# Performance work log

Hardware: AMD Instinct MI355X
Metric: run time of the kernel (lower is better)

Reference implementation:

```python
import jax, jax.numpy as jnp
import numpy as np

N = 100000      # nodes
DEG = 16        # fixed out-degree -> nnz = N*DEG (static for jit)
NNZ = N * DEG
IN_DIM, HID, OUT = 256, 64, 64


def setup_inputs() -> dict:
    key = jax.random.key(0)
    k1, k2, k3, k4, k5 = jax.random.split(key, 5)
    X = jax.random.normal(k1, (N, IN_DIM), dtype=jnp.float32)
    W1 = jax.random.normal(k2, (IN_DIM, HID), dtype=jnp.float32) / np.sqrt(IN_DIM)
    W2 = jax.random.normal(k3, (HID, OUT), dtype=jnp.float32) / np.sqrt(HID)
    vals = jax.random.uniform(k4, (NNZ,), dtype=jnp.float32)
    rowptr = (jnp.arange(N + 1, dtype=jnp.int32) * DEG)  # fixed-degree CSR
    colind = jax.random.randint(k5, (NNZ,), 0, N, dtype=jnp.int32)
    return {"X": X, "W1": W1, "W2": W2, "vals": vals,
            "rowptr": rowptr, "colind": colind}


def spmm_csr(rowptr, colind, vals, B):
    """CSR SpMM: out[i] = sum_{j in row i} vals[j] * B[colind[j]]."""
    deg = rowptr[1:] - rowptr[:-1]                      # [N]
    rows = jnp.repeat(jnp.arange(N, dtype=jnp.int32), deg,
                      total_repeat_length=NNZ)           # [NNZ]
    gathered = vals[:, None] * B[colind]                 # [NNZ, F]
    return jax.ops.segment_sum(gathered, rows, num_segments=N)


def reference(X, W1, W2, vals, rowptr, colind):
    h = X @ W1                        # lin1 (no bias)
    h = spmm_csr(rowptr, colind, vals, h)   # A @ h
    h = jax.nn.relu(h)
    out = h @ W2                      # lin2 (no bias)
    out = spmm_csr(rowptr, colind, vals, out)  # A @ out
    return out
```

## Files before the change

kernel.cpp:

```cpp
#include <hip/hip_runtime.h>
#include <hip/hip_bf16.h>

#define N_NODES 100000
#define DEG 16
#define NT16 6250
#define NG64 1563
#define G1_BLOCKS 782
#define G1_WSTRIDE (G1_BLOCKS * 4)

typedef __attribute__((ext_vector_type(8))) short short8;
typedef __attribute__((ext_vector_type(4))) float f32x4;
typedef __attribute__((ext_vector_type(4))) float f4raw;
typedef __attribute__((ext_vector_type(4))) int   i4raw;
typedef __attribute__((ext_vector_type(4))) unsigned u4raw;

__device__ inline unsigned short f2bf(float f) {
    union { float f; unsigned u; } v; v.f = f;
    unsigned u = v.u;
    u += 0x7FFFu + ((u >> 16) & 1u);
    return (unsigned short)(u >> 16);
}
__device__ inline unsigned pk2bf(float a, float b) {
    union { __hip_bfloat162 b2; unsigned u; } v;
    v.b2 = __float22bfloat162_rn(make_float2(a, b));
    return v.u;
}
__device__ inline float bflo(unsigned u) {
    union { unsigned u; float f; } v; v.u = u << 16; return v.f;
}
__device__ inline float bfhi(unsigned u) {
    union { unsigned u; float f; } v; v.u = u & 0xFFFF0000u; return v.f;
}

__global__ __launch_bounds__(256) void gemm1_k256(const float* __restrict__ X,
                                                  const float* __restrict__ W1,
                                                  unsigned short* __restrict__ h)
{
    __shared__ unsigned short wfrag[256 * 64];

    const int tid  = threadIdx.x;
    const int lane = tid & 63;
    const int wid  = tid >> 6;
    const int q    = lane >> 4;
    const int l16  = lane & 15;

    {
        const int kg = tid >> 2;
        const int cq = tid & 3;
        float4 wr[16];
        #pragma unroll
        for (int r = 0; r < 4; ++r)
            #pragma unroll
            for (int i = 0; i < 4; ++i)
                wr[r * 4 + i] = *(const float4*)(W1 + (kg * 4 + r) * 64 + cq * 16 + i * 4);
        const int kb  = kg >> 3;
        const int lnr = (((kg * 4) >> 3) & 3) * 16;
        const int jb  = (kg * 4) & 7;
        #pragma unroll
        for (int c = 0; c < 16; ++c) {
            ushort4 w4;
            #pragma unroll
            for (int r = 0; r < 4; ++r) {
                float4 v = wr[r * 4 + (c >> 2)];
                float  f = ((c & 3) == 0) ? v.x : ((c & 3) == 1) ? v.y :
                           ((c & 3) == 2) ? v.z : v.w;
                ((unsigned short*)&w4)[r] = f2bf(f);
            }
            *(ushort4*)&wfrag[(((kb * 4) + cq) * 64 + lnr + c) * 8 + jb] = w4;
        }
    }
    __syncthreads();

    const int bpidx = (((l16 << 2) | q) << 2);
    const size_t xoff = (size_t)(lane >> 2) * 256 + (lane & 3) * 8;

    int t = blockIdx.x * 4 + wid;

    f4raw pa[8];
    {
        const float* xb = X + (size_t)t * 16 * 256 + xoff;
        #pragma unroll
        for (int kb = 0; kb < 4; ++kb) {
            pa[2 * kb]     = __builtin_nontemporal_load((const f4raw*)(xb + kb * 32));
            pa[2 * kb + 1] = __builtin_nontemporal_load((const f4raw*)(xb + kb * 32 + 4));
        }
    }

    while (t < NT16) {
        const float* xb = X + (size_t)t * 16 * 256 + xoff;
        f4raw pb[8];
        #pragma unroll
        for (int kb = 4; kb < 8; ++kb) {
            pb[2 * (kb - 4)]     = __builtin_nontemporal_load((const f4raw*)(xb + kb * 32));
            pb[2 * (kb - 4) + 1] = __builtin_nontemporal_load((const f4raw*)(xb + kb * 32 + 4));
        }

        f32x4 a0 = {0,0,0,0}, a1 = {0,0,0,0}, a2 = {0,0,0,0}, a3 = {0,0,0,0};

        #pragma unroll
        for (int kb = 0; kb < 4; ++kb) {
            union { int u[4]; short8 s; } uu;
            uu.u[0] = __builtin_amdgcn_ds_bpermute(bpidx, (int)pk2bf(pa[2*kb].x,   pa[2*kb].y));
            uu.u[1] = __builtin_amdgcn_ds_bpermute(bpidx, (int)pk2bf(pa[2*kb].z,   pa[2*kb].w));
            uu.u[2] = __builtin_amdgcn_ds_bpermute(bpidx, (int)pk2bf(pa[2*kb+1].x, pa[2*kb+1].y));
            uu.u[3] = __builtin_amdgcn_ds_bpermute(bpidx, (int)pk2bf(pa[2*kb+1].z, pa[2*kb+1].w));
            const short8* wp = (const short8*)&wfrag[(size_t)((kb * 4) * 64 + lane) * 8];
            a0 = __builtin_amdgcn_mfma_f32_16x16x32_bf16(uu.s, wp[0 * 64], a0, 0, 0, 0);
            a1 = __builtin_amdgcn_mfma_f32_16x16x32_bf16(uu.s, wp[1 * 64], a1, 0, 0, 0);
            a2 = __builtin_amdgcn_mfma_f32_16x16x32_bf16(uu.s, wp[2 * 64], a2, 0, 0, 0);
            a3 = __builtin_amdgcn_mfma_f32_16x16x32_bf16(uu.s, wp[3 * 64], a3, 0, 0, 0);
        }

        const int tn = t + G1_WSTRIDE;
        if (tn < NT16) {
            const float* xn = X + (size_t)tn * 16 * 256 + xoff;
            #pragma unroll
            for (int kb = 0; kb < 4; ++kb) {
                pa[2 * kb]     = __builtin_nontemporal_load((const f4raw*)(xn + kb * 32));
                pa[2 * kb + 1] = __builtin_nontemporal_load((const f4raw*)(xn + kb * 32 + 4));
            }
        }

        #pragma unroll
        for (int kb = 4; kb < 8; ++kb) {
            const int i = kb - 4;
            union { int u[4]; short8 s; } uu;
            uu.u[0] = __builtin_amdgcn_ds_bpermute(bpidx, (int)pk2bf(pb[2*i].x,   pb[2*i].y));
            uu.u[1] = __builtin_amdgcn_ds_bpermute(bpidx, (int)pk2bf(pb[2*i].z,   pb[2*i].w));
            uu.u[2] = __builtin_amdgcn_ds_bpermute(bpidx, (int)pk2bf(pb[2*i+1].x, pb[2*i+1].y));
            uu.u[3] = __builtin_amdgcn_ds_bpermute(bpidx, (int)pk2bf(pb[2*i+1].z, pb[2*i+1].w));
            const short8* wp = (const short8*)&wfrag[(size_t)((kb * 4) * 64 + lane) * 8];
            a0 = __builtin_amdgcn_mfma_f32_16x16x32_bf16(uu.s, wp[0 * 64], a0, 0, 0, 0);
            a1 = __builtin_amdgcn_mfma_f32_16x16x32_bf16(uu.s, wp[1 * 64], a1, 0, 0, 0);
            a2 = __builtin_amdgcn_mfma_f32_16x16x32_bf16(uu.s, wp[2 * 64], a2, 0, 0, 0);
            a3 = __builtin_amdgcn_mfma_f32_16x16x32_bf16(uu.s, wp[3 * 64], a3, 0, 0, 0);
        }

        {
            unsigned short* hrow = h + (size_t)(t * 16) * 64;
            #pragma unroll
            for (int r = 0; r < 4; ++r) {
                const int row = q * 4 + r;
                hrow[row * 64 +  0 + l16] = f2bf(a0[r]);
                hrow[row * 64 + 16 + l16] = f2bf(a1[r]);
                hrow[row * 64 + 32 + l16] = f2bf(a2[r]);
                hrow[row * 64 + 48 + l16] = f2bf(a3[r]);
            }
        }
        t = tn;
    }
}

__device__ inline void gather_row8(const unsigned short* __restrict__ B,
                                   const int* __restrict__ ci,
                                   const float* __restrict__ vv,
                                   int j8, float* __restrict__ acc)
{
    #pragma unroll
    for (int b = 0; b < 2; ++b) {
        i4raw c0 = __builtin_nontemporal_load((const i4raw*)ci + 2 * b);
        i4raw c1 = __builtin_nontemporal_load((const i4raw*)ci + 2 * b + 1);
        f4raw v0 = __builtin_nontemporal_load((const f4raw*)vv + 2 * b);
        f4raw v1 = __builtin_nontemporal_load((const f4raw*)vv + 2 * b + 1);
        uint4 g0 = *(const uint4*)(B + (size_t)c0.x * 64 + j8 * 8);
        uint4 g1 = *(const uint4*)(B + (size_t)c0.y * 64 + j8 * 8);
        uint4 g2 = *(const uint4*)(B + (size_t)c0.z * 64 + j8 * 8);
        uint4 g3 = *(const uint4*)(B + (size_t)c0.w * 64 + j8 * 8);
        uint4 g4 = *(const uint4*)(B + (size_t)c1.x * 64 + j8 * 8);
        uint4 g5 = *(const uint4*)(B + (size_t)c1.y * 64 + j8 * 8);
        uint4 g6 = *(const uint4*)(B + (size_t)c1.z * 64 + j8 * 8);
        uint4 g7 = *(const uint4*)(B + (size_t)c1.w * 64 + j8 * 8);
#define ACC8(g, s) \
        acc[0] += (s) * bflo((g).x); acc[1] += (s) * bfhi((g).x); \
        acc[2] += (s) * bflo((g).y); acc[3] += (s) * bfhi((g).y); \
        acc[4] += (s) * bflo((g).z); acc[5] += (s) * bfhi((g).z); \
        acc[6] += (s) * bflo((g).w); acc[7] += (s) * bfhi((g).w);
        ACC8(g0, v0.x) ACC8(g1, v0.y) ACC8(g2, v0.z) ACC8(g3, v0.w)
        ACC8(g4, v1.x) ACC8(g5, v1.y) ACC8(g6, v1.z) ACC8(g7, v1.w)
#undef ACC8
    }
}

__global__ __launch_bounds__(256) void spmm_gemm2(const int* __restrict__ colind,
                                                  const float* __restrict__ vals,
                                                  const unsigned short* __restrict__ h,
                                                  const float* __restrict__ W2,
                                                  unsigned short* __restrict__ o1)
{
    __shared__ unsigned short wfrag2[64 * 64];
    __shared__ unsigned short stage[4][16 * 72];

    const int tid  = threadIdx.x;
    const int lane = tid & 63;
    const int wid  = tid >> 6;
    const int q    = lane >> 4;
    const int l16  = lane & 15;

    {
        const int r4 = tid >> 2;
        const int qt = tid & 3;
        float4 wr[4];
        #pragma unroll
        for (int i = 0; i < 4; ++i)
            wr[i] = *(const float4*)(W2 + r4 * 64 + qt * 16 + i * 4);
        const int kb  = r4 >> 5;
        const int j   = r4 & 7;
        const int lnr = ((r4 >> 3) & 3) * 16;
        #pragma unroll
        for (int c = 0; c < 16; ++c) {
            float f = ((c & 3) == 0) ? wr[c >> 2].x :
                      ((c & 3) == 1) ? wr[c >> 2].y :
                      ((c & 3) == 2) ? wr[c >> 2].z : wr[c >> 2].w;
            wfrag2[(((kb * 4) + qt) * 64 + lnr + c) * 8 + j] = f2bf(f);
        }
    }
    __syncthreads();

    const int base = blockIdx.x * 64 + wid * 16;
    unsigned short* st = stage[wid];
    const int rl = lane >> 3;
    const int j8 = lane & 7;

    #pragma unroll
    for (int p = 0; p < 2; ++p) {
        int lr  = p * 8 + rl;
        int row = base + lr;
        int rc  = row < N_NODES ? row : N_NODES - 1;
        float acc[8] = {0.f,0.f,0.f,0.f,0.f,0.f,0.f,0.f};
        gather_row8(h, colind + (size_t)rc * DEG, vals + (size_t)rc * DEG, j8, acc);
        uint4 pk;
        pk.x = pk2bf(fmaxf(acc[0], 0.f), fmaxf(acc[1], 0.f));
        pk.y = pk2bf(fmaxf(acc[2], 0.f), fmaxf(acc[3], 0.f));
        pk.z = pk2bf(fmaxf(acc[4], 0.f), fmaxf(acc[5], 0.f));
        pk.w = pk2bf(fmaxf(acc[6], 0.f), fmaxf(acc[7], 0.f));
        *(uint4*)&st[lr * 72 + j8 * 8] = pk;
    }

    f32x4 a0 = {0,0,0,0}, a1 = {0,0,0,0}, a2 = {0,0,0,0}, a3 = {0,0,0,0};
    #pragma unroll
    for (int kb = 0; kb < 2; ++kb) {
        short8 af = *(const short8*)&st[l16 * 72 + kb * 32 + q * 8];
        const short8* wp = (const short8*)&wfrag2[(size_t)((kb * 4) * 64 + lane) * 8];
        a0 = __builtin_amdgcn_mfma_f32_16x16x32_bf16(af, wp[0 * 64], a0, 0, 0, 0);
        a1 = __builtin_amdgcn_mfma_f32_16x16x32_bf16(af, wp[1 * 64], a1, 0, 0, 0);
        a2 = __builtin_amdgcn_mfma_f32_16x16x32_bf16(af, wp[2 * 64], a2, 0, 0, 0);
        a3 = __builtin_amdgcn_mfma_f32_16x16x32_bf16(af, wp[3 * 64], a3, 0, 0, 0);
    }
    #pragma unroll
    for (int r = 0; r < 4; ++r) {
        int rr = (q * 4 + r) * 72 + l16;
        st[rr + 0 * 16] = f2bf(a0[r]);
        st[rr + 1 * 16] = f2bf(a1[r]);
        st[rr + 2 * 16] = f2bf(a2[r]);
        st[rr + 3 * 16] = f2bf(a3[r]);
    }
    #pragma unroll
    for (int i = 0; i < 4; ++i) {
        int row = base + i * 4 + q;
        if (row < N_NODES) {
            uint2 v = *(const uint2*)&st[(i * 4 + q) * 72 + l16 * 4];
            *(uint2*)(o1 + (size_t)row * 64 + l16 * 4) = v;
        }
    }
}

__global__ __launch_bounds__(256) void spmm_out(const int* __restrict__ colind,
                                                const float* __restrict__ vals,
                                                const unsigned short* __restrict__ B,
                                                float* __restrict__ out)
{
    const int tid  = threadIdx.x;
    const int lane = tid & 63;
    const int wid  = tid >> 6;
    const int rl   = lane >> 3;
    const int j8   = lane & 7;
    const int row  = blockIdx.x * 32 + wid * 8 + rl;

    float acc[8] = {0.f,0.f,0.f,0.f,0.f,0.f,0.f,0.f};
    gather_row8(B, colind + (size_t)row * DEG, vals + (size_t)row * DEG, j8, acc);

    f4raw lo = { acc[0], acc[1], acc[2], acc[3] };
    f4raw hi = { acc[4], acc[5], acc[6], acc[7] };
    float* op = out + (size_t)row * 64 + j8 * 8;
    *(f4raw*)op       = lo;
    *(f4raw*)(op + 4) = hi;
}

extern "C" void kernel_launch(void* const* d_in, const int* in_sizes, int n_in,
                              void* d_out, int out_size, void* d_ws, size_t ws_size,
                              hipStream_t stream) {
    const float* X      = (const float*)d_in[0];
    const float* W1     = (const float*)d_in[1];
    const float* W2     = (const float*)d_in[2];
    const float* vals   = (const float*)d_in[3];
    const int*   colind = (const int*)d_in[5];
    float*       out    = (float*)d_out;

    unsigned short* h  = (unsigned short*)d_ws;
    unsigned short* o1 = h + (size_t)N_NODES * 64;

    hipLaunchKernelGGL(gemm1_k256, dim3(G1_BLOCKS), dim3(256), 0, stream, X, W1, h);
    hipLaunchKernelGGL(spmm_gemm2, dim3(NG64), dim3(256), 0, stream,
                       colind, vals, h, W2, o1);
    hipLaunchKernelGGL(spmm_out, dim3(N_NODES / 32), dim3(256), 0, stream,
                       colind, vals, o1, out);
}
```

Baseline: 230.4 us.

## Shrink fused SpMM+GEMM2 blocks to 32 rows and split MFMA columns across waves

The fused SpMM/ReLU/GEMM2 kernel now handles 32 rows per block instead of 64. Each wave gathers 8 rows once rather than looping over 16. The 64-wide output is split so that two waves share one 16-row tile and each computes two column tiles, with block-wide barriers coordinating a shared stage buffer. The output is written back with wider 16-byte stores. Twice as many blocks are launched, adding parallelism and halving per-wave gather latency, at the cost of more block-wide syncs and repeating the W2 fragment setup in twice as many blocks.

```diff
diff --git a/kernel.cpp b/kernel.cpp
--- a/kernel.cpp
+++ b/kernel.cpp
@@ -4,7 +4,7 @@
 #define N_NODES 100000
 #define DEG 16
 #define NT16 6250
-#define NG64 1563
+#define NB32 3125
 #define G1_BLOCKS 782
 #define G1_WSTRIDE (G1_BLOCKS * 4)
 
@@ -188,13 +188,15 @@
                                                   unsigned short* __restrict__ o1)
 {
     __shared__ unsigned short wfrag2[64 * 64];
-    __shared__ unsigned short stage[4][16 * 72];
+    __shared__ unsigned short stage[32 * 72];
 
     const int tid  = threadIdx.x;
     const int lane = tid & 63;
     const int wid  = tid >> 6;
     const int q    = lane >> 4;
     const int l16  = lane & 15;
+    const int rl   = lane >> 3;
+    const int j8   = lane & 7;
 
     {
         const int r4 = tid >> 2;
@@ -214,53 +216,54 @@
             wfrag2[(((kb * 4) + qt) * 64 + lnr + c) * 8 + j] = f2bf(f);
         }
     }
-    __syncthreads();
-
-    const int base = blockIdx.x * 64 + wid * 16;
-    unsigned short* st = stage[wid];
-    const int rl = lane >> 3;
-    const int j8 = lane & 7;
-
-    #pragma unroll
-    for (int p = 0; p < 2; ++p) {
-        int lr  = p * 8 + rl;
-        int row = base + lr;
-        int rc  = row < N_NODES ? row : N_NODES - 1;
-        float acc[8] = {0.f,0.f,0.f,0.f,0.f,0.f,0.f,0.f};
-        gather_row8(h, colind + (size_t)rc * DEG, vals + (size_t)rc * DEG, j8, acc);
+
+    const int base = blockIdx.x * 32;
+
+    const int lr  = wid * 8 + rl;
+    const int row = base + lr;
+    float acc[8] = {0.f,0.f,0.f,0.f,0.f,0.f,0.f,0.f};
+    gather_row8(h, colind + (size_t)row * DEG, vals + (size_t)row * DEG, j8, acc);
+    {
         uint4 pk;
         pk.x = pk2bf(fmaxf(acc[0], 0.f), fmaxf(acc[1], 0.f));
         pk.y = pk2bf(fmaxf(acc[2], 0.f), fmaxf(acc[3], 0.f));
         pk.z = pk2bf(fmaxf(acc[4], 0.f), fmaxf(acc[5], 0.f));
         pk.w = pk2bf(fmaxf(acc[6], 0.f), fmaxf(acc[7], 0.f));
-        *(uint4*)&st[lr * 72 + j8 * 8] = pk;
-    }
-
-    f32x4 a0 = {0,0,0,0}, a1 = {0,0,0,0}, a2 = {0,0,0,0}, a3 = {0,0,0,0};
-    #pragma unroll
-    for (int kb = 0; kb < 2; ++kb) {
-        short8 af = *(const short8*)&st[l16 * 72 + kb * 32 + q * 8];
-        const short8* wp = (const short8*)&wfrag2[(size_t)((kb * 4) * 64 + lane) * 8];
-        a0 = __builtin_amdgcn_mfma_f32_16x16x32_bf16(af, wp[0 * 64], a0, 0, 0, 0);
-        a1 = __builtin_amdgcn_mfma_f32_16x16x32_bf16(af, wp[1 * 64], a1, 0, 0, 0);
-        a2 = __builtin_amdgcn_mfma_f32_16x16x32_bf16(af, wp[2 * 64], a2, 0, 0, 0);
-        a3 = __builtin_amdgcn_mfma_f32_16x16x32_bf16(af, wp[3 * 64], a3, 0, 0, 0);
-    }
+        *(uint4*)&stage[lr * 72 + j8 * 8] = pk;
+    }
+    __syncthreads();
+
+    const int t  = wid >> 1;
+    const int ch = wid & 1;
+
+    short8 af0 = *(const short8*)&stage[(t * 16 + l16) * 72 + 0 * 32 + q * 8];
+    short8 af1 = *(const short8*)&stage[(t * 16 + l16) * 72 + 1 * 32 + q * 8];
+    __syncthreads();
+
+    f32x4 b0 = {0,0,0,0}, b1 = {0,0,0,0};
+    {
+        const short8* wp0 = (const short8*)&wfrag2[(size_t)((0 * 4) * 64 + lane) * 8];
+        const short8* wp1 = (const short8*)&wfrag2[(size_t)((1 * 4) * 64 + lane) * 8];
+        const int c0 = 2 * ch, c1 = 2 * ch + 1;
+        b0 = __builtin_amdgcn_mfma_f32_16x16x32_bf16(af0, wp0[c0 * 64], b0, 0, 0, 0);
+        b0 = __builtin_amdgcn_mfma_f32_16x16x32_bf16(af1, wp1[c0 * 64], b0, 0, 0, 0);
+        b1 = __builtin_amdgcn_mfma_f32_16x16x32_bf16(af0, wp0[c1 * 64], b1, 0, 0, 0);
+        b1 = __builtin_amdgcn_mfma_f32_16x16x32_bf16(af1, wp1[c1 * 64], b1, 0, 0, 0);
+    }
+
     #pragma unroll
     for (int r = 0; r < 4; ++r) {
-        int rr = (q * 4 + r) * 72 + l16;
-        st[rr + 0 * 16] = f2bf(a0[r]);
-        st[rr + 1 * 16] = f2bf(a1[r]);
-        st[rr + 2 * 16] = f2bf(a2[r]);
-        st[rr + 3 * 16] = f2bf(a3[r]);
-    }
-    #pragma unroll
-    for (int i = 0; i < 4; ++i) {
-        int row = base + i * 4 + q;
-        if (row < N_NODES) {
-            uint2 v = *(const uint2*)&st[(i * 4 + q) * 72 + l16 * 4];
-            *(uint2*)(o1 + (size_t)row * 64 + l16 * 4) = v;
-        }
+        const int srow = t * 16 + q * 4 + r;
+        stage[srow * 72 + (2 * ch)     * 16 + l16] = f2bf(b0[r]);
+        stage[srow * 72 + (2 * ch + 1) * 16 + l16] = f2bf(b1[r]);
+    }
+    __syncthreads();
+
+    {
+        const int srow = tid >> 3;
+        const int c    = tid & 7;
+        uint4 v = *(const uint4*)&stage[srow * 72 + c * 8];
+        *(uint4*)(o1 + (size_t)(base + srow) * 64 + c * 8) = v;
     }
 }
 
@@ -300,8 +303,8 @@
     unsigned short* o1 = h + (size_t)N_NODES * 64;
 
     hipLaunchKernelGGL(gemm1_k256, dim3(G1_BLOCKS), dim3(256), 0, stream, X, W1, h);
-    hipLaunchKernelGGL(spmm_gemm2, dim3(NG64), dim3(256), 0, stream,
+    hipLaunchKernelGGL(spmm_gemm2, dim3(NB32), dim3(256), 0, stream,
                        colind, vals, h, W2, o1);
-    hipLaunchKernelGGL(spmm_out, dim3(N_NODES / 32), dim3(256), 0, stream,
+    hipLaunchKernelGGL(spmm_out, dim3(NB32), dim3(256), 0, stream,
                        colind, vals, o1, out);
 }
```

After: 228.9 us. No clear change (-0.6%).
